# Optimization experiments

Measured on AMD Instinct MI355X. Metric: run time of the kernel, lower is better.

Reference implementation:

```python
import jax, jax.numpy as jnp
import numpy as np

B, L, D, H, M = 4, 2048, 256, 8, 256
HEAD = D // H
EPS = 1e-6


def _pos_embedding(maxlen, d):
    i = np.arange(maxlen, dtype=np.float64)[:, None]
    j = np.arange(d, dtype=np.float64)[None, :]
    angle = i / np.power(10000.0, (j - (j % 2)) / d)
    pe = np.where(j % 2 == 0, np.sin(angle), np.cos(angle))
    return jnp.asarray(pe, jnp.float32)  # [L, D]


def _projection_matrix(m, d, seed=0):
    # FAVOR+ orthogonal random features: one full QR block (m == d here),
    # rows rescaled by norms of iid Gaussian rows (scaling=0 in source).
    rng = np.random.default_rng(seed)
    block = rng.standard_normal((d, d))
    q, _ = np.linalg.qr(block)
    q = q.T[:m]
    mult = np.linalg.norm(rng.standard_normal((m, d)), axis=1)
    return jnp.asarray(mult[:, None] * q, jnp.float32)  # [M, D]


def _softmax_kernel(x, is_query, proj):
    # x: [B, L, H, D], proj: [M, D]
    d = x.shape[-1]
    m = proj.shape[0]
    x = x * (float(d) ** -0.25)
    xp = jnp.einsum('blhd,md->blhm', x, proj)
    diag = 0.5 * jnp.sum(x * x, axis=-1, keepdims=True)
    if is_query:
        mx = jnp.max(xp, axis=-1, keepdims=True)
    else:
        mx = jnp.max(xp, axis=(-3, -1), keepdims=True)  # over L and M
    return (float(m) ** -0.5) * (jnp.exp(xp - diag - mx) + EPS)


def setup_inputs() -> dict:
    key = jax.random.key(0)
    ks = jax.random.split(key, 12)
    s = 1.0 / np.sqrt(D)
    inp = {
        'query': jax.random.normal(ks[0], (B, L, D), jnp.float32),
        'key': jax.random.normal(ks[1], (B, L, D), jnp.float32),
        'value': jax.random.normal(ks[2], (B, L, D), jnp.float32),
        'mask': jnp.ones((B, L), jnp.float32),
        'Wq': jax.random.normal(ks[3], (D, D), jnp.float32) * s,
        'bq': jnp.zeros((D,), jnp.float32),
        'Wk': jax.random.normal(ks[4], (D, D), jnp.float32) * s,
        'bk': jnp.zeros((D,), jnp.float32),
        'Wv': jax.random.normal(ks[5], (D, D), jnp.float32) * s,
        'bv': jnp.zeros((D,), jnp.float32),
        'Wo': jax.random.normal(ks[6], (D, D), jnp.float32) * s,
        'bo': jnp.zeros((D,), jnp.float32),
        'proj': _projection_matrix(M, D, seed=0),
        'pos': _pos_embedding(L, D),
    }
    return inp


def reference(query, key, value, mask, Wq, bq, Wk, bk, Wv, bv, Wo, bo, proj, pos):
    b = query.shape[0]
    q = query @ Wq + bq                      # [B, L, D]
    k = key @ Wk + bk
    v = value @ Wv + bv
    # per-head copies keep the FULL model_size feature dim (as in source)
    q = jnp.broadcast_to(q[:, :, None, :], (b, L, H, D))
    k = jnp.broadcast_to(k[:, :, None, :], (b, L, H, D))
    pos_b = pos[None]                        # [1, L, D]
    cos_pos = jnp.repeat(pos_b[..., None, 1::2], 2, axis=-1)  # [1, L, 1, D]
    sin_pos = jnp.repeat(pos_b[..., None, ::2], 2, axis=-1)

    def rot(x):
        x2 = jnp.stack([-x[..., 1::2], x[..., ::2]], axis=-1).reshape(x.shape)
        return x * cos_pos + x2 * sin_pos

    q = rot(q)
    k = rot(k)
    v = v.reshape(b, L, H, HEAD)

    qp = _softmax_kernel(q, True, proj)      # [B, L, H, M]
    kp = _softmax_kernel(k, False, proj)     # [B, L, H, M]

    kvs = jnp.einsum('blhm,blhd->bhmd', kp, v)
    num = jnp.einsum('blhm,bhmd->blhd', qp, kvs)
    den = jnp.einsum('blhm,bhm->blh', qp, jnp.sum(kp, axis=1))
    ctx = (num / den[..., None]).reshape(b, L, D)
    return ctx @ Wo + bo
```

## Files before the change

### kernel.cpp

```cpp
#include <hip/hip_runtime.h>

typedef unsigned short u16;
typedef unsigned int u32;
typedef __bf16 bf16x8 __attribute__((ext_vector_type(8)));
typedef float f32x4 __attribute__((ext_vector_type(4)));

__device__ __forceinline__ float bf2f(u16 u) { return __uint_as_float(((u32)u) << 16); }
__device__ __forceinline__ u16 f2bf(float f) {
  u32 x = __float_as_uint(f);
  x += 0x7fffu + ((x >> 16) & 1u);
  return (u16)(x >> 16);
}
__device__ __forceinline__ u32 encf(float x) {
  u32 u = __float_as_uint(x);
  return (u >> 31) ? ~u : (u | 0x80000000u);
}
__device__ __forceinline__ float decf(u32 e) {
  return (e >> 31) ? __uint_as_float(e & 0x7fffffffu) : __uint_as_float(~e);
}

#define MFMA(a, b, c) __builtin_amdgcn_mfma_f32_16x16x32_bf16(a, b, c, 0, 0, 0)

__global__ __launch_bounds__(256) void prep_w(
    const float* Wq, const float* Wk, const float* Wv, const float* Wo,
    const float* proj, const float* bv,
    u16* WqT, u16* WkT, u16* projb, u16* WWT, float* bw,
    float* __restrict__ ksum, u32* __restrict__ mxk) {
  __shared__ u16 tsh[32][33];
  __shared__ u16 As[64][40];
  __shared__ u16 Bs[64][40];
  const int z = blockIdx.z;
  const int x = threadIdx.x, y = threadIdx.y;
  const int tid = y * 32 + x;
  if (z < 2) {
    const float* s = z == 0 ? Wq : Wk;
    u16* d = z == 0 ? WqT : WkT;
    int r0 = blockIdx.y * 32, c0 = blockIdx.x * 32;
#pragma unroll
    for (int i = 0; i < 32; i += 8) tsh[y + i][x] = f2bf(s[(r0 + y + i) * 256 + c0 + x]);
    __syncthreads();
#pragma unroll
    for (int i = 0; i < 32; i += 8) d[(c0 + y + i) * 256 + r0 + x] = tsh[x][y + i];
    return;
  }
  if (z == 2) {
    int r0 = blockIdx.y * 32, c0 = blockIdx.x * 32;
#pragma unroll
    for (int i = 0; i < 32; i += 8)
      projb[(r0 + y + i) * 256 + c0 + x] = f2bf(proj[(r0 + y + i) * 256 + c0 + x]);
    return;
  }
  if (blockIdx.x < 4 && blockIdx.y < 4) {
    const int o0 = blockIdx.x * 64, i0 = blockIdx.y * 64;
    const int lane = tid & 63, wid = tid >> 6;
    const int wm = (wid >> 1) * 32, wn = (wid & 1) * 32;
    const int fm = lane & 15, fq = (lane >> 4) * 8, rowq = (lane >> 4) * 4;
    const int dr = tid >> 3, oc = (tid & 7) * 8;
    const int ir = tid >> 2, dc = (tid & 3) * 8;
    f32x4 acc[2][2] = {};
    for (int it = 0; it < 8; ++it) {
      int d0 = it * 32;
      float4 w0 = *(const float4*)(Wo + (d0 + dr) * 256 + o0 + oc);
      float4 w1 = *(const float4*)(Wo + (d0 + dr) * 256 + o0 + oc + 4);
      float4 v0 = *(const float4*)(Wv + (i0 + ir) * 256 + d0 + dc);
      float4 v1 = *(const float4*)(Wv + (i0 + ir) * 256 + d0 + dc + 4);
      __syncthreads();
      float wv[8] = {w0.x, w0.y, w0.z, w0.w, w1.x, w1.y, w1.z, w1.w};
#pragma unroll
      for (int j = 0; j < 8; ++j) As[oc + j][dr] = f2bf(wv[j]);
      u16* bp = &Bs[ir][dc];
      bp[0] = f2bf(v0.x); bp[1] = f2bf(v0.y); bp[2] = f2bf(v0.z); bp[3] = f2bf(v0.w);
      bp[4] = f2bf(v1.x); bp[5] = f2bf(v1.y); bp[6] = f2bf(v1.z); bp[7] = f2bf(v1.w);
      __syncthreads();
      bf16x8 a0 = *(const bf16x8*)&As[wm + fm][fq];
      bf16x8 a1 = *(const bf16x8*)&As[wm + 16 + fm][fq];
      bf16x8 b0 = *(const bf16x8*)&Bs[wn + fm][fq];
      bf16x8 b1 = *(const bf16x8*)&Bs[wn + 16 + fm][fq];
      acc[0][0] = MFMA(a0, b0, acc[0][0]);
      acc[0][1] = MFMA(a0, b1, acc[0][1]);
      acc[1][0] = MFMA(a1, b0, acc[1][0]);
      acc[1][1] = MFMA(a1, b1, acc[1][1]);
    }
#pragma unroll
    for (int mt = 0; mt < 2; ++mt)
#pragma unroll
      for (int nt = 0; nt < 2; ++nt)
#pragma unroll
        for (int r = 0; r < 4; ++r)
          WWT[(o0 + wm + mt * 16 + rowq + r) * 256 + i0 + wn + nt * 16 + fm] =
              f2bf(acc[mt][nt][r]);
    return;
  }
  if (blockIdx.x == 4 && blockIdx.y == 0) {
    float s = 0.0f;
    for (int d = 0; d < 256; ++d) s = fmaf(bv[d], Wo[d * 256 + tid], s);
    bw[tid] = s;
    for (int i = tid; i < 1024; i += 256) ksum[i] = 0.0f;
    if (tid < 4) mxk[tid] = 0u;
  }
}

__global__ __launch_bounds__(256, 2) void projrot2(
    const float* __restrict__ Xq, const float* __restrict__ Xk,
    const u16* __restrict__ WqT, const u16* __restrict__ WkT,
    const float* __restrict__ bq, const float* __restrict__ bk,
    const float* __restrict__ pos, const u16* __restrict__ projb,
    float* __restrict__ diag_k, u16* __restrict__ qp,
    float* __restrict__ xp, u32* __restrict__ mxk) {
  const int mode = blockIdx.z;
  const float* X = mode ? Xq : Xk;
  const u16* W = mode ? WqT : WkT;
  const float* bias = mode ? bq : bk;
  __shared__ u16 As[2][32][40];
  __shared__ u16 Bs[2][256][40];
  __shared__ u16 cbuf[32][264];
  __shared__ float dred[2][32];
  __shared__ float mred[2][32];
  __shared__ float wred[4];
  const int row0 = blockIdx.x * 32;
  const int t = threadIdx.x;
  const int lane = t & 63, wid = t >> 6;
  const int wrow = wid & 1, wcol = wid >> 1;
  const int fm = lane & 15, fq = (lane >> 4) * 8, rowq = (lane >> 4) * 4;
  const int ar = t >> 3, ak = (t & 7) * 4;

  const float* Xr = X + (long long)(row0 + ar) * 256;
  const u16* Wr = W + (long long)t * 256;
  float4 av = *(const float4*)(Xr + ak);
  uint4 bv0 = ((const uint4*)Wr)[0];
  uint4 bv1 = ((const uint4*)Wr)[1];
  uint4 bv2 = ((const uint4*)Wr)[2];
  uint4 bv3 = ((const uint4*)Wr)[3];
  As[0][ar][ak] = f2bf(av.x); As[0][ar][ak + 1] = f2bf(av.y);
  As[0][ar][ak + 2] = f2bf(av.z); As[0][ar][ak + 3] = f2bf(av.w);
  { uint4* bsp = (uint4*)&Bs[0][t][0]; bsp[0] = bv0; bsp[1] = bv1; bsp[2] = bv2; bsp[3] = bv3; }
  av = *(const float4*)(Xr + 32 + ak);
  { const uint4* wn = (const uint4*)(Wr + 32); bv0 = wn[0]; bv1 = wn[1]; bv2 = wn[2]; bv3 = wn[3]; }
  __syncthreads();
  f32x4 acc[8] = {};
  for (int s = 0; s < 8; ++s) {
    const int cur = s & 1;
    float4 av2; uint4 nb0, nb1, nb2, nb3;
    if (s < 6) {
      av2 = *(const float4*)(Xr + (s + 2) * 32 + ak);
      const uint4* wn = (const uint4*)(Wr + (s + 2) * 32);
      nb0 = wn[0]; nb1 = wn[1]; nb2 = wn[2]; nb3 = wn[3];
    }
    bf16x8 af = *(const bf16x8*)&As[cur][wrow * 16 + fm][fq];
#pragma unroll
    for (int j = 0; j < 8; ++j) {
      bf16x8 bf = *(const bf16x8*)&Bs[cur][wcol * 128 + j * 16 + fm][fq];
      acc[j] = MFMA(af, bf, acc[j]);
    }
    if (s < 7) {
      const int nxt = cur ^ 1;
      As[nxt][ar][ak] = f2bf(av.x); As[nxt][ar][ak + 1] = f2bf(av.y);
      As[nxt][ar][ak + 2] = f2bf(av.z); As[nxt][ar][ak + 3] = f2bf(av.w);
      uint4* bsp = (uint4*)&Bs[nxt][t][0];
      bsp[0] = bv0; bsp[1] = bv1; bsp[2] = bv2; bsp[3] = bv3;
      if (s < 6) { av = av2; bv0 = nb0; bv1 = nb1; bv2 = nb2; bv3 = nb3; }
      __syncthreads();
    }
  }

  float dsum[4] = {};
#pragma unroll
  for (int j = 0; j < 8; ++j) {
    float bb2 = bias[wcol * 128 + j * 16 + fm];
#pragma unroll
    for (int r = 0; r < 4; ++r) {
      float v = acc[j][r] + bb2;
      acc[j][r] = v;
      dsum[r] += v * v;
    }
  }
#pragma unroll
  for (int o = 1; o < 16; o <<= 1)
#pragma unroll
    for (int r = 0; r < 4; ++r) dsum[r] += __shfl_xor(dsum[r], o, 64);
  if (fm == 0) {
#pragma unroll
    for (int r = 0; r < 4; ++r) dred[wcol][wrow * 16 + rowq + r] = dsum[r];
  }
  __syncthreads();
  if (mode == 0 && t < 32) diag_k[row0 + t] = 0.03125f * (dred[0][t] + dred[1][t]);

#pragma unroll
  for (int j = 0; j < 8; ++j) {
    const int c = wcol * 128 + j * 16 + fm;
#pragma unroll
    for (int r = 0; r < 4; ++r) {
      const int row = wrow * 16 + rowq + r;
      const int l = (row0 + row) & 2047;
      float v = acc[j][r];
      float prt = __shfl_xor(v, 1, 64);
      float x2 = (fm & 1) ? prt : -prt;
      float2 cs = *(const float2*)(pos + (long long)l * 256 + (c & ~1));
      cbuf[row][c] = f2bf(0.25f * (v * cs.y + x2 * cs.x));
    }
  }

  const u16* Pr = projb + (long long)t * 256;
  uint4 pv0 = ((const uint4*)Pr)[0];
  uint4 pv1 = ((const uint4*)Pr)[1];
  uint4 pv2 = ((const uint4*)Pr)[2];
  uint4 pv3 = ((const uint4*)Pr)[3];
  { uint4* bsp = (uint4*)&Bs[0][t][0]; bsp[0] = pv0; bsp[1] = pv1; bsp[2] = pv2; bsp[3] = pv3; }
  { const uint4* pn = (const uint4*)(Pr + 32); pv0 = pn[0]; pv1 = pn[1]; pv2 = pn[2]; pv3 = pn[3]; }
  __syncthreads();
  f32x4 acc2[8] = {};
  for (int s = 0; s < 8; ++s) {
    const int cur = s & 1;
    uint4 np0, np1, np2, np3;
    if (s < 6) {
      const uint4* pn = (const uint4*)(Pr + (s + 2) * 32);
      np0 = pn[0]; np1 = pn[1]; np2 = pn[2]; np3 = pn[3];
    }
    bf16x8 af = *(const bf16x8*)&cbuf[wrow * 16 + fm][s * 32 + fq];
#pragma unroll
    for (int j = 0; j < 8; ++j) {
      bf16x8 bf = *(const bf16x8*)&Bs[cur][wcol * 128 + j * 16 + fm][fq];
      acc2[j] = MFMA(af, bf, acc2[j]);
    }
    if (s < 7) {
      const int nxt = cur ^ 1;
      uint4* bsp = (uint4*)&Bs[nxt][t][0];
      bsp[0] = pv0; bsp[1] = pv1; bsp[2] = pv2; bsp[3] = pv3;
      if (s < 6) { pv0 = np0; pv1 = np1; pv2 = np2; pv3 = np3; }
      __syncthreads();
    }
  }

  if (mode == 1) {
    float m4[4] = {-3.0e38f, -3.0e38f, -3.0e38f, -3.0e38f};
#pragma unroll
    for (int j = 0; j < 8; ++j)
#pragma unroll
      for (int r = 0; r < 4; ++r) m4[r] = fmaxf(m4[r], acc2[j][r]);
#pragma unroll
    for (int o = 1; o < 16; o <<= 1)
#pragma unroll
      for (int r = 0; r < 4; ++r) m4[r] = fmaxf(m4[r], __shfl_xor(m4[r], o, 64));
    if (fm == 0) {
#pragma unroll
      for (int r = 0; r < 4; ++r) mred[wcol][wrow * 16 + rowq + r] = m4[r];
    }
    __syncthreads();
#pragma unroll
    for (int j = 0; j < 8; ++j) {
      const int col = wcol * 128 + j * 16 + fm;
#pragma unroll
      for (int r = 0; r < 4; ++r) {
        const int row = wrow * 16 + rowq + r;
        float mxr = fmaxf(mred[0][row], mred[1][row]);
        float dgr = 0.03125f * (dred[0][row] + dred[1][row]);
        float v = 0.0625f * (__expf(acc2[j][r] - dgr - mxr) + 1e-6f);
        qp[(long long)(row0 + row) * 256 + col] = f2bf(v);
      }
    }
  } else {
    float mx = -3.0e38f;
#pragma unroll
    for (int j = 0; j < 8; ++j) {
      int col = wcol * 128 + j * 16 + fm;
#pragma unroll
      for (int r = 0; r < 4; ++r) {
        float v = acc2[j][r];
        xp[(long long)(row0 + wrow * 16 + rowq + r) * 256 + col] = v;
        mx = fmaxf(mx, v);
      }
    }
#pragma unroll
    for (int o = 32; o > 0; o >>= 1) mx = fmaxf(mx, __shfl_xor(mx, o, 64));
    if (lane == 0) wred[wid] = mx;
    __syncthreads();
    if (t == 0) {
      float m = fmaxf(fmaxf(wred[0], wred[1]), fmaxf(wred[2], wred[3]));
      atomicMax(mxk + (row0 >> 11), encf(m));
    }
  }
}

__global__ __launch_bounds__(256, 2) void kvs_raw_split(
    const float* __restrict__ xp, const float* __restrict__ Xv,
    const float* __restrict__ diag_k, const u32* __restrict__ mxk,
    float* __restrict__ part, float* __restrict__ ksum) {
  __shared__ u16 As[2][64][40];
  __shared__ u16 Bs[2][64][40];
  __shared__ float ksbuf[32][65];
  const int mxt = blockIdx.x, ny = blockIdx.y, z = blockIdx.z;
  const int b = z >> 3, kc = z & 7;
  const long long l0 = (long long)b * 2048 + kc * 256;
  const int t = threadIdx.x;
  const int lane = t & 63, wid = t >> 6;
  const int wrow = wid >> 1, wcol = wid & 1;
  const int fm = lane & 15, rowq = (lane >> 4) * 4;
  const float mxv = decf(mxk[b]);
  const int sr = t >> 3, sc = (t & 7) * 8;
  const int pcol = (((sr >> 3) ^ (t & 3)) << 3) + (sr & 7);
  const int g = lane >> 4;
  const int arow0 = wrow * 32 + fm, arow1 = arow0 + 16;
  const int brow0 = wcol * 32 + fm, brow1 = brow0 + 16;
  const int apg0 = (g ^ ((arow0 >> 3) & 3)) << 3;
  const int apg1 = (g ^ ((arow1 >> 3) & 3)) << 3;
  const int bpg0 = (g ^ ((brow0 >> 3) & 3)) << 3;
  const int bpg1 = (g ^ ((brow1 >> 3) & 3)) << 3;
  f32x4 acc[2][2] = {};
  float ksp[8] = {};
  long long lrow = l0 + sr;
  float4 x0 = *(const float4*)(xp + lrow * 256 + mxt * 64 + sc);
  float4 x1 = *(const float4*)(xp + lrow * 256 + mxt * 64 + sc + 4);
  float4 v0 = *(const float4*)(Xv + lrow * 256 + ny * 64 + sc);
  float4 v1 = *(const float4*)(Xv + lrow * 256 + ny * 64 + sc + 4);
  float dgl = diag_k[lrow];
  {
    float xv[8] = {x0.x, x0.y, x0.z, x0.w, x1.x, x1.y, x1.z, x1.w};
    float vv[8] = {v0.x, v0.y, v0.z, v0.w, v1.x, v1.y, v1.z, v1.w};
#pragma unroll
    for (int j = 0; j < 8; ++j) {
      float f = 0.0625f * (__expf(xv[j] - dgl - mxv) + 1e-6f);
      u16 kb = f2bf(f);
      As[0][sc + j][pcol] = kb;
      ksp[j] += bf2f(kb);
      Bs[0][sc + j][pcol] = f2bf(vv[j]);
    }
  }
  lrow = l0 + 32 + sr;
  x0 = *(const float4*)(xp + lrow * 256 + mxt * 64 + sc);
  x1 = *(const float4*)(xp + lrow * 256 + mxt * 64 + sc + 4);
  v0 = *(const float4*)(Xv + lrow * 256 + ny * 64 + sc);
  v1 = *(const float4*)(Xv + lrow * 256 + ny * 64 + sc + 4);
  dgl = diag_k[lrow];
  __syncthreads();
  for (int s = 0; s < 8; ++s) {
    const int cur = s & 1;
    float4 nx0, nx1, nv0, nv1; float ndg;
    if (s < 6) {
      long long lr2 = l0 + (s + 2) * 32 + sr;
      nx0 = *(const float4*)(xp + lr2 * 256 + mxt * 64 + sc);
      nx1 = *(const float4*)(xp + lr2 * 256 + mxt * 64 + sc + 4);
      nv0 = *(const float4*)(Xv + lr2 * 256 + ny * 64 + sc);
      nv1 = *(const float4*)(Xv + lr2 * 256 + ny * 64 + sc + 4);
      ndg = diag_k[lr2];
    }
    bf16x8 a0 = *(const bf16x8*)&As[cur][arow0][apg0];
    bf16x8 a1 = *(const bf16x8*)&As[cur][arow1][apg1];
    bf16x8 b0 = *(const bf16x8*)&Bs[cur][brow0][bpg0];
    bf16x8 b1 = *(const bf16x8*)&Bs[cur][brow1][bpg1];
    acc[0][0] = MFMA(a0, b0, acc[0][0]);
    acc[0][1] = MFMA(a0, b1, acc[0][1]);
    acc[1][0] = MFMA(a1, b0, acc[1][0]);
    acc[1][1] = MFMA(a1, b1, acc[1][1]);
    if (s < 7) {
      const int nxt = cur ^ 1;
      float xv[8] = {x0.x, x0.y, x0.z, x0.w, x1.x, x1.y, x1.z, x1.w};
      float vv[8] = {v0.x, v0.y, v0.z, v0.w, v1.x, v1.y, v1.z, v1.w};
#pragma unroll
      for (int j = 0; j < 8; ++j) {
        float f = 0.0625f * (__expf(xv[j] - dgl - mxv) + 1e-6f);
        u16 kb = f2bf(f);
        As[nxt][sc + j][pcol] = kb;
        ksp[j] += bf2f(kb);
        Bs[nxt][sc + j][pcol] = f2bf(vv[j]);
      }
      if (s < 6) { x0 = nx0; x1 = nx1; v0 = nv0; v1 = nv1; dgl = ndg; }
      __syncthreads();
    }
  }
#pragma unroll
  for (int mt = 0; mt < 2; ++mt)
#pragma unroll
    for (int nt = 0; nt < 2; ++nt)
#pragma unroll
      for (int r = 0; r < 4; ++r)
        part[(long long)z * 65536 +
             (long long)(mxt * 64 + wrow * 32 + mt * 16 + rowq + r) * 256 +
             ny * 64 + wcol * 32 + nt * 16 + fm] = acc[mt][nt][r];
#pragma unroll
  for (int j = 0; j < 8; ++j) ksbuf[sr][sc + j] = ksp[j];
  __syncthreads();
  if (ny == 0 && t < 64) {
    float ssum = 0.0f;
    for (int r = 0; r < 32; ++r) ssum += ksbuf[r][t];
    atomicAdd(ksum + b * 256 + mxt * 64 + t, ssum);
  }
}

__global__ __launch_bounds__(256) void kvsw(
    const u16* __restrict__ WWT, const float* __restrict__ part,
    const float* __restrict__ ksum, const float* __restrict__ bw,
    u16* __restrict__ kvsWT) {
  __shared__ u16 As[2][64][40];
  __shared__ u16 Bs[2][16][40];
  const int bid = blockIdx.x;
  const int b = bid >> 6;
  const int o0 = ((bid >> 4) & 3) * 64;
  const int m0 = (bid & 15) * 16;
  const int t = threadIdx.x;
  const int w4 = t >> 6;
  const int lane = t & 63;
  const int fm = lane & 15, fq = (lane >> 4) * 8, rowq = (lane >> 4) * 4;
  const int arow = t >> 2, acol = (t & 3) * 8;
  const int brow = t >> 4, bcol = (t & 15) * 2;
  const float* pbase = part + (long long)(b * 8) * 65536 + (m0 + brow) * 256 + bcol;
  f32x4 acc = {0.0f, 0.0f, 0.0f, 0.0f};
  uint4 av = *(const uint4*)(WWT + (o0 + arow) * 256 + acol);
  float2 ps[8];
#pragma unroll
  for (int kc = 0; kc < 8; ++kc) ps[kc] = *(const float2*)(pbase + (long long)kc * 65536);
  {
    float sx = ps[0].x + ps[1].x + ps[2].x + ps[3].x + ps[4].x + ps[5].x + ps[6].x + ps[7].x;
    float sy = ps[0].y + ps[1].y + ps[2].y + ps[3].y + ps[4].y + ps[5].y + ps[6].y + ps[7].y;
    *(uint4*)&As[0][arow][acol] = av;
    Bs[0][brow][bcol] = f2bf(sx);
    Bs[0][brow][bcol + 1] = f2bf(sy);
  }
  av = *(const uint4*)(WWT + (o0 + arow) * 256 + 32 + acol);
#pragma unroll
  for (int kc = 0; kc < 8; ++kc) ps[kc] = *(const float2*)(pbase + (long long)kc * 65536 + 32);
  __syncthreads();
  for (int s = 0; s < 8; ++s) {
    const int cur = s & 1;
    uint4 nav; float2 nps[8];
    if (s < 6) {
      const int k2 = (s + 2) * 32;
      nav = *(const uint4*)(WWT + (o0 + arow) * 256 + k2 + acol);
#pragma unroll
      for (int kc = 0; kc < 8; ++kc) nps[kc] = *(const float2*)(pbase + (long long)kc * 65536 + k2);
    }
    bf16x8 af = *(const bf16x8*)&As[cur][w4 * 16 + fm][fq];
    bf16x8 bf = *(const bf16x8*)&Bs[cur][fm][fq];
    acc = MFMA(af, bf, acc);
    if (s < 7) {
      const int nxt = cur ^ 1;
      float sx = ps[0].x + ps[1].x + ps[2].x + ps[3].x + ps[4].x + ps[5].x + ps[6].x + ps[7].x;
      float sy = ps[0].y + ps[1].y + ps[2].y + ps[3].y + ps[4].y + ps[5].y + ps[6].y + ps[7].y;
      *(uint4*)&As[nxt][arow][acol] = av;
      Bs[nxt][brow][bcol] = f2bf(sx);
      Bs[nxt][brow][bcol + 1] = f2bf(sy);
      if (s < 6) {
        av = nav;
#pragma unroll
        for (int kc = 0; kc < 8; ++kc) ps[kc] = nps[kc];
      }
      __syncthreads();
    }
  }
  const int col = m0 + fm;
  float ksv = ksum[b * 256 + col];
#pragma unroll
  for (int r = 0; r < 4; ++r) {
    int row = o0 + w4 * 16 + rowq + r;
    kvsWT[(long long)b * 65536 + (long long)row * 256 + col] =
        f2bf(acc[r] + bw[row] * ksv);
  }
}

__global__ __launch_bounds__(256, 2) void numout(
    const u16* __restrict__ qp, const float* __restrict__ ksum,
    const u16* __restrict__ kvsWT, const float* __restrict__ bo,
    float* __restrict__ out) {
  __shared__ u16 As[2][16][40];
  __shared__ u16 Bs[2][256][40];
  __shared__ float ksm[256], dsh[16];
  const int row0 = blockIdx.x * 16;
  const int b = blockIdx.z;
  const long long qrow = (long long)b * 2048 + row0;
  const int t = threadIdx.x;
  const int lane = t & 63, wid = t >> 6;
  const int fm = lane & 15, fq = (lane >> 4) * 8, rowq = (lane >> 4) * 4;
  const int ar = t >> 4, ak = (t & 15) * 2;

  const u16* qa = qp + (qrow + ar) * 256;
  const u16* kvr = kvsWT + (long long)b * 65536 + (long long)t * 256;

  u32 a0 = *(const u32*)(qa + ak);
  uint4 bv0 = ((const uint4*)kvr)[0];
  uint4 bv1 = ((const uint4*)kvr)[1];
  uint4 bv2 = ((const uint4*)kvr)[2];
  uint4 bv3 = ((const uint4*)kvr)[3];
  *(u32*)&As[0][ar][ak] = a0;
  { uint4* bsp = (uint4*)&Bs[0][t][0]; bsp[0] = bv0; bsp[1] = bv1; bsp[2] = bv2; bsp[3] = bv3; }
  a0 = *(const u32*)(qa + 32 + ak);
  { const uint4* kn = (const uint4*)(kvr + 32); bv0 = kn[0]; bv1 = kn[1]; bv2 = kn[2]; bv3 = kn[3]; }

  ksm[t] = ksum[b * 256 + t];
  const int prow = t >> 4, pc0 = (t & 15) * 16;
  const u16* qr = qp + (qrow + prow) * 256 + pc0;
  uint4 u0 = *(const uint4*)(qr);
  uint4 u1 = *(const uint4*)(qr + 8);
  __syncthreads();

  float denp = 0.0f;
  u32 uu[8] = {u0.x, u0.y, u0.z, u0.w, u1.x, u1.y, u1.z, u1.w};
#pragma unroll
  for (int j = 0; j < 8; ++j) {
    denp += bf2f((u16)(uu[j] & 0xffffu)) * ksm[pc0 + 2 * j];
    denp += bf2f((u16)(uu[j] >> 16)) * ksm[pc0 + 2 * j + 1];
  }
#pragma unroll
  for (int o = 1; o < 16; o <<= 1) denp += __shfl_xor(denp, o, 64);
  if ((t & 15) == 0) dsh[prow] = denp;

  f32x4 acc[4] = {};
  for (int s = 0; s < 8; ++s) {
    const int cur = s & 1;
    u32 na0; uint4 nb0, nb1, nb2, nb3;
    if (s < 6) {
      const int k2 = (s + 2) * 32;
      na0 = *(const u32*)(qa + k2 + ak);
      const uint4* kn = (const uint4*)(kvr + k2);
      nb0 = kn[0]; nb1 = kn[1]; nb2 = kn[2]; nb3 = kn[3];
    }
    bf16x8 af = *(const bf16x8*)&As[cur][fm][fq];
#pragma unroll
    for (int j = 0; j < 4; ++j) {
      bf16x8 bf = *(const bf16x8*)&Bs[cur][wid * 64 + j * 16 + fm][fq];
      acc[j] = MFMA(af, bf, acc[j]);
    }
    if (s < 7) {
      const int nxt = cur ^ 1;
      *(u32*)&As[nxt][ar][ak] = a0;
      uint4* bsp = (uint4*)&Bs[nxt][t][0];
      bsp[0] = bv0; bsp[1] = bv1; bsp[2] = bv2; bsp[3] = bv3;
      if (s < 6) { a0 = na0; bv0 = nb0; bv1 = nb1; bv2 = nb2; bv3 = nb3; }
      __syncthreads();
    }
  }
#pragma unroll
  for (int j = 0; j < 4; ++j) {
    int col = wid * 64 + j * 16 + fm;
    float bb2 = bo[col];
#pragma unroll
    for (int r = 0; r < 4; ++r) {
      int l = rowq + r;
      out[(qrow + l) * 256 + col] = acc[j][r] / dsh[l] + bb2;
    }
  }
}

extern "C" void kernel_launch(void* const* d_in, const int* in_sizes, int n_in,
                              void* d_out, int out_size, void* d_ws, size_t ws_size,
                              hipStream_t stream) {
  (void)in_sizes; (void)n_in; (void)out_size; (void)ws_size;
  const float* query = (const float*)d_in[0];
  const float* key = (const float*)d_in[1];
  const float* value = (const float*)d_in[2];
  const float* Wq = (const float*)d_in[4];
  const float* bq = (const float*)d_in[5];
  const float* Wk = (const float*)d_in[6];
  const float* bk = (const float*)d_in[7];
  const float* Wv = (const float*)d_in[8];
  const float* bv = (const float*)d_in[9];
  const float* Wo = (const float*)d_in[10];
  const float* bo = (const float*)d_in[11];
  const float* proj = (const float*)d_in[12];
  const float* pos = (const float*)d_in[13];

  char* w = (char*)d_ws;
  u16* qp = (u16*)(w);
  float* xp = (float*)(w + (4 << 20));
  float* part = (float*)(w + (12 << 20));
  u16* kvsWT = (u16*)(w + (20 << 20));
  u16* WqT = (u16*)(w + (21 << 20));
  u16* WkT = WqT + 65536;
  u16* projb = WkT + 65536;
  u16* WWT = projb + 65536;
  float* diag_k = (float*)(w + (22 << 20));
  float* ksum = diag_k + 8192;
  float* bw = ksum + 1024;
  u32* mxk = (u32*)(bw + 256);

  prep_w<<<dim3(8, 8, 4), dim3(32, 8), 0, stream>>>(Wq, Wk, Wv, Wo, proj, bv,
                                                    WqT, WkT, projb, WWT, bw,
                                                    ksum, mxk);
  projrot2<<<dim3(256, 1, 2), dim3(256), 0, stream>>>(
      query, key, WqT, WkT, bq, bk, pos, projb, diag_k, qp, xp, mxk);
  kvs_raw_split<<<dim3(4, 4, 32), dim3(256), 0, stream>>>(xp, value, diag_k, mxk,
                                                          part, ksum);
  kvsw<<<dim3(256), dim3(256), 0, stream>>>(WWT, part, ksum, bw, kvsWT);
  numout<<<dim3(128, 1, 4), dim3(256), 0, stream>>>(qp, ksum, kvsWT, bo,
                                                    (float*)d_out);
}
```

Measured before the change: 66.57 us.

## Apply fused Wv·Wo to value rows before KV accumulation instead of after

The value projection, pre-multiplied by Wo (WWT), is now applied directly to the value rows as a third mode of the projection kernel and stored as bf16. The KV-state kernel then contracts the key features with these pre-transformed values, with operand roles swapped. The separate kvsw GEMM is replaced by a simple reduction over the split partials plus the bias term. This removes one small GEMM launch and halves the value-read bandwidth through bf16, but it adds a full L×D×D GEMM per batch and an extra bf16 rounding step on the values.

```diff
diff --git a/kernel.cpp b/kernel.cpp
--- a/kernel.cpp
+++ b/kernel.cpp
@@ -102,15 +102,14 @@
 
 __global__ __launch_bounds__(256, 2) void projrot2(
     const float* __restrict__ Xq, const float* __restrict__ Xk,
+    const float* __restrict__ Xv,
     const u16* __restrict__ WqT, const u16* __restrict__ WkT,
+    const u16* __restrict__ WWT,
     const float* __restrict__ bq, const float* __restrict__ bk,
     const float* __restrict__ pos, const u16* __restrict__ projb,
     float* __restrict__ diag_k, u16* __restrict__ qp,
-    float* __restrict__ xp, u32* __restrict__ mxk) {
+    float* __restrict__ xp, u16* __restrict__ xvw, u32* __restrict__ mxk) {
   const int mode = blockIdx.z;
-  const float* X = mode ? Xq : Xk;
-  const u16* W = mode ? WqT : WkT;
-  const float* bias = mode ? bq : bk;
   __shared__ u16 As[2][32][40];
   __shared__ u16 Bs[2][256][40];
   __shared__ u16 cbuf[32][264];
@@ -123,6 +122,9 @@
   const int wrow = wid & 1, wcol = wid >> 1;
   const int fm = lane & 15, fq = (lane >> 4) * 8, rowq = (lane >> 4) * 4;
   const int ar = t >> 3, ak = (t & 7) * 4;
+
+  const float* X = mode == 0 ? Xk : (mode == 1 ? Xq : Xv);
+  const u16* W = mode == 0 ? WkT : (mode == 1 ? WqT : WWT);
 
   const float* Xr = X + (long long)(row0 + ar) * 256;
   const u16* Wr = W + (long long)t * 256;
@@ -163,6 +165,18 @@
     }
   }
 
+  if (mode == 2) {
+#pragma unroll
+    for (int j = 0; j < 8; ++j) {
+      const int col = wcol * 128 + j * 16 + fm;
+#pragma unroll
+      for (int r = 0; r < 4; ++r)
+        xvw[(long long)(row0 + wrow * 16 + rowq + r) * 256 + col] = f2bf(acc[j][r]);
+    }
+    return;
+  }
+
+  const float* bias = mode ? bq : bk;
   float dsum[4] = {};
 #pragma unroll
   for (int j = 0; j < 8; ++j) {
@@ -282,13 +296,13 @@
 }
 
 __global__ __launch_bounds__(256, 2) void kvs_raw_split(
-    const float* __restrict__ xp, const float* __restrict__ Xv,
+    const float* __restrict__ xp, const u16* __restrict__ xvw,
     const float* __restrict__ diag_k, const u32* __restrict__ mxk,
     float* __restrict__ part, float* __restrict__ ksum) {
   __shared__ u16 As[2][64][40];
   __shared__ u16 Bs[2][64][40];
   __shared__ float ksbuf[32][65];
-  const int mxt = blockIdx.x, ny = blockIdx.y, z = blockIdx.z;
+  const int ox = blockIdx.x, my = blockIdx.y, z = blockIdx.z;
   const int b = z >> 3, kc = z & 7;
   const long long l0 = (long long)b * 2048 + kc * 256;
   const int t = threadIdx.x;
@@ -308,39 +322,39 @@
   f32x4 acc[2][2] = {};
   float ksp[8] = {};
   long long lrow = l0 + sr;
-  float4 x0 = *(const float4*)(xp + lrow * 256 + mxt * 64 + sc);
-  float4 x1 = *(const float4*)(xp + lrow * 256 + mxt * 64 + sc + 4);
-  float4 v0 = *(const float4*)(Xv + lrow * 256 + ny * 64 + sc);
-  float4 v1 = *(const float4*)(Xv + lrow * 256 + ny * 64 + sc + 4);
+  uint4 va = *(const uint4*)(xvw + lrow * 256 + ox * 64 + sc);
+  float4 x0 = *(const float4*)(xp + lrow * 256 + my * 64 + sc);
+  float4 x1 = *(const float4*)(xp + lrow * 256 + my * 64 + sc + 4);
   float dgl = diag_k[lrow];
   {
+    u16 a8[8] = {(u16)(va.x & 0xffffu), (u16)(va.x >> 16),
+                 (u16)(va.y & 0xffffu), (u16)(va.y >> 16),
+                 (u16)(va.z & 0xffffu), (u16)(va.z >> 16),
+                 (u16)(va.w & 0xffffu), (u16)(va.w >> 16)};
     float xv[8] = {x0.x, x0.y, x0.z, x0.w, x1.x, x1.y, x1.z, x1.w};
-    float vv[8] = {v0.x, v0.y, v0.z, v0.w, v1.x, v1.y, v1.z, v1.w};
 #pragma unroll
     for (int j = 0; j < 8; ++j) {
+      As[0][sc + j][pcol] = a8[j];
       float f = 0.0625f * (__expf(xv[j] - dgl - mxv) + 1e-6f);
       u16 kb = f2bf(f);
-      As[0][sc + j][pcol] = kb;
+      Bs[0][sc + j][pcol] = kb;
       ksp[j] += bf2f(kb);
-      Bs[0][sc + j][pcol] = f2bf(vv[j]);
     }
   }
   lrow = l0 + 32 + sr;
-  x0 = *(const float4*)(xp + lrow * 256 + mxt * 64 + sc);
-  x1 = *(const float4*)(xp + lrow * 256 + mxt * 64 + sc + 4);
-  v0 = *(const float4*)(Xv + lrow * 256 + ny * 64 + sc);
-  v1 = *(const float4*)(Xv + lrow * 256 + ny * 64 + sc + 4);
+  va = *(const uint4*)(xvw + lrow * 256 + ox * 64 + sc);
+  x0 = *(const float4*)(xp + lrow * 256 + my * 64 + sc);
+  x1 = *(const float4*)(xp + lrow * 256 + my * 64 + sc + 4);
   dgl = diag_k[lrow];
   __syncthreads();
   for (int s = 0; s < 8; ++s) {
     const int cur = s & 1;
-    float4 nx0, nx1, nv0, nv1; float ndg;
+    uint4 nva; float4 nx0, nx1; float ndg;
     if (s < 6) {
       long long lr2 = l0 + (s + 2) * 32 + sr;
-      nx0 = *(const float4*)(xp + lr2 * 256 + mxt * 64 + sc);
-      nx1 = *(const float4*)(xp + lr2 * 256 + mxt * 64 + sc + 4);
-      nv0 = *(const float4*)(Xv + lr2 * 256 + ny * 64 + sc);
-      nv1 = *(const float4*)(Xv + lr2 * 256 + ny * 64 + sc + 4);
+      nva = *(const uint4*)(xvw + lr2 * 256 + ox * 64 + sc);
+      nx0 = *(const float4*)(xp + lr2 * 256 + my * 64 + sc);
+      nx1 = *(const float4*)(xp + lr2 * 256 + my * 64 + sc + 4);
       ndg = diag_k[lr2];
     }
     bf16x8 a0 = *(const bf16x8*)&As[cur][arow0][apg0];
@@ -353,17 +367,20 @@
     acc[1][1] = MFMA(a1, b1, acc[1][1]);
     if (s < 7) {
       const int nxt = cur ^ 1;
+      u16 a8[8] = {(u16)(va.x & 0xffffu), (u16)(va.x >> 16),
+                   (u16)(va.y & 0xffffu), (u16)(va.y >> 16),
+                   (u16)(va.z & 0xffffu), (u16)(va.z >> 16),
+                   (u16)(va.w & 0xffffu), (u16)(va.w >> 16)};
       float xv[8] = {x0.x, x0.y, x0.z, x0.w, x1.x, x1.y, x1.z, x1.w};
-      float vv[8] = {v0.x, v0.y, v0.z, v0.w, v1.x, v1.y, v1.z, v1.w};
 #pragma unroll
       for (int j = 0; j < 8; ++j) {
+        As[nxt][sc + j][pcol] = a8[j];
         float f = 0.0625f * (__expf(xv[j] - dgl - mxv) + 1e-6f);
         u16 kb = f2bf(f);
-        As[nxt][sc + j][pcol] = kb;
+        Bs[nxt][sc + j][pcol] = kb;
         ksp[j] += bf2f(kb);
-        Bs[nxt][sc + j][pcol] = f2bf(vv[j]);
       }
-      if (s < 6) { x0 = nx0; x1 = nx1; v0 = nv0; v1 = nv1; dgl = ndg; }
+      if (s < 6) { va = nva; x0 = nx0; x1 = nx1; dgl = ndg; }
       __syncthreads();
     }
   }
@@ -374,85 +391,34 @@
 #pragma unroll
       for (int r = 0; r < 4; ++r)
         part[(long long)z * 65536 +
-             (long long)(mxt * 64 + wrow * 32 + mt * 16 + rowq + r) * 256 +
-             ny * 64 + wcol * 32 + nt * 16 + fm] = acc[mt][nt][r];
+             (long long)(ox * 64 + wrow * 32 + mt * 16 + rowq + r) * 256 +
+             my * 64 + wcol * 32 + nt * 16 + fm] = acc[mt][nt][r];
 #pragma unroll
   for (int j = 0; j < 8; ++j) ksbuf[sr][sc + j] = ksp[j];
   __syncthreads();
-  if (ny == 0 && t < 64) {
+  if (ox == 0 && t < 64) {
     float ssum = 0.0f;
     for (int r = 0; r < 32; ++r) ssum += ksbuf[r][t];
-    atomicAdd(ksum + b * 256 + mxt * 64 + t, ssum);
-  }
-}
-
-__global__ __launch_bounds__(256) void kvsw(
-    const u16* __restrict__ WWT, const float* __restrict__ part,
-    const float* __restrict__ ksum, const float* __restrict__ bw,
-    u16* __restrict__ kvsWT) {
-  __shared__ u16 As[2][64][40];
-  __shared__ u16 Bs[2][16][40];
-  const int bid = blockIdx.x;
-  const int b = bid >> 6;
-  const int o0 = ((bid >> 4) & 3) * 64;
-  const int m0 = (bid & 15) * 16;
+    atomicAdd(ksum + b * 256 + my * 64 + t, ssum);
+  }
+}
+
+__global__ __launch_bounds__(256) void kvsred(
+    const float* __restrict__ part, const float* __restrict__ ksum,
+    const float* __restrict__ bw, u16* __restrict__ kvsWT) {
+  const int b = blockIdx.z;
+  const int o0 = blockIdx.x * 4;
   const int t = threadIdx.x;
-  const int w4 = t >> 6;
-  const int lane = t & 63;
-  const int fm = lane & 15, fq = (lane >> 4) * 8, rowq = (lane >> 4) * 4;
-  const int arow = t >> 2, acol = (t & 3) * 8;
-  const int brow = t >> 4, bcol = (t & 15) * 2;
-  const float* pbase = part + (long long)(b * 8) * 65536 + (m0 + brow) * 256 + bcol;
-  f32x4 acc = {0.0f, 0.0f, 0.0f, 0.0f};
-  uint4 av = *(const uint4*)(WWT + (o0 + arow) * 256 + acol);
-  float2 ps[8];
-#pragma unroll
-  for (int kc = 0; kc < 8; ++kc) ps[kc] = *(const float2*)(pbase + (long long)kc * 65536);
-  {
-    float sx = ps[0].x + ps[1].x + ps[2].x + ps[3].x + ps[4].x + ps[5].x + ps[6].x + ps[7].x;
-    float sy = ps[0].y + ps[1].y + ps[2].y + ps[3].y + ps[4].y + ps[5].y + ps[6].y + ps[7].y;
-    *(uint4*)&As[0][arow][acol] = av;
-    Bs[0][brow][bcol] = f2bf(sx);
-    Bs[0][brow][bcol + 1] = f2bf(sy);
-  }
-  av = *(const uint4*)(WWT + (o0 + arow) * 256 + 32 + acol);
-#pragma unroll
-  for (int kc = 0; kc < 8; ++kc) ps[kc] = *(const float2*)(pbase + (long long)kc * 65536 + 32);
-  __syncthreads();
-  for (int s = 0; s < 8; ++s) {
-    const int cur = s & 1;
-    uint4 nav; float2 nps[8];
-    if (s < 6) {
-      const int k2 = (s + 2) * 32;
-      nav = *(const uint4*)(WWT + (o0 + arow) * 256 + k2 + acol);
-#pragma unroll
-      for (int kc = 0; kc < 8; ++kc) nps[kc] = *(const float2*)(pbase + (long long)kc * 65536 + k2);
-    }
-    bf16x8 af = *(const bf16x8*)&As[cur][w4 * 16 + fm][fq];
-    bf16x8 bf = *(const bf16x8*)&Bs[cur][fm][fq];
-    acc = MFMA(af, bf, acc);
-    if (s < 7) {
-      const int nxt = cur ^ 1;
-      float sx = ps[0].x + ps[1].x + ps[2].x + ps[3].x + ps[4].x + ps[5].x + ps[6].x + ps[7].x;
-      float sy = ps[0].y + ps[1].y + ps[2].y + ps[3].y + ps[4].y + ps[5].y + ps[6].y + ps[7].y;
-      *(uint4*)&As[nxt][arow][acol] = av;
-      Bs[nxt][brow][bcol] = f2bf(sx);
-      Bs[nxt][brow][bcol + 1] = f2bf(sy);
-      if (s < 6) {
-        av = nav;
-#pragma unroll
-        for (int kc = 0; kc < 8; ++kc) ps[kc] = nps[kc];
-      }
-      __syncthreads();
-    }
-  }
-  const int col = m0 + fm;
-  float ksv = ksum[b * 256 + col];
-#pragma unroll
-  for (int r = 0; r < 4; ++r) {
-    int row = o0 + w4 * 16 + rowq + r;
-    kvsWT[(long long)b * 65536 + (long long)row * 256 + col] =
-        f2bf(acc[r] + bw[row] * ksv);
+  const float ksv = ksum[b * 256 + t];
+#pragma unroll
+  for (int o = 0; o < 4; ++o) {
+    const int orow = o0 + o;
+    const float* pb = part + (long long)(b * 8) * 65536 + (long long)orow * 256 + t;
+    float s = 0.0f;
+#pragma unroll
+    for (int kc = 0; kc < 8; ++kc) s += pb[(long long)kc * 65536];
+    kvsWT[(long long)b * 65536 + (long long)orow * 256 + t] =
+        f2bf(s + bw[orow] * ksv);
   }
 }
 
@@ -560,13 +526,14 @@
   char* w = (char*)d_ws;
   u16* qp = (u16*)(w);
   float* xp = (float*)(w + (4 << 20));
-  float* part = (float*)(w + (12 << 20));
-  u16* kvsWT = (u16*)(w + (20 << 20));
-  u16* WqT = (u16*)(w + (21 << 20));
+  u16* xvw = (u16*)(w + (12 << 20));
+  float* part = (float*)(w + (16 << 20));
+  u16* kvsWT = (u16*)(w + (24 << 20));
+  u16* WqT = (u16*)(w + (25 << 20));
   u16* WkT = WqT + 65536;
   u16* projb = WkT + 65536;
   u16* WWT = projb + 65536;
-  float* diag_k = (float*)(w + (22 << 20));
+  float* diag_k = (float*)(w + (26 << 20));
   float* ksum = diag_k + 8192;
   float* bw = ksum + 1024;
   u32* mxk = (u32*)(bw + 256);
@@ -574,11 +541,12 @@
   prep_w<<<dim3(8, 8, 4), dim3(32, 8), 0, stream>>>(Wq, Wk, Wv, Wo, proj, bv,
                                                     WqT, WkT, projb, WWT, bw,
                                                     ksum, mxk);
-  projrot2<<<dim3(256, 1, 2), dim3(256), 0, stream>>>(
-      query, key, WqT, WkT, bq, bk, pos, projb, diag_k, qp, xp, mxk);
-  kvs_raw_split<<<dim3(4, 4, 32), dim3(256), 0, stream>>>(xp, value, diag_k, mxk,
+  projrot2<<<dim3(256, 1, 3), dim3(256), 0, stream>>>(
+      query, key, value, WqT, WkT, WWT, bq, bk, pos, projb, diag_k, qp, xp,
+      xvw, mxk);
+  kvs_raw_split<<<dim3(4, 4, 32), dim3(256), 0, stream>>>(xp, xvw, diag_k, mxk,
                                                           part, ksum);
-  kvsw<<<dim3(256), dim3(256), 0, stream>>>(WWT, part, ksum, bw, kvsWT);
+  kvsred<<<dim3(64, 1, 4), dim3(256), 0, stream>>>(part, ksum, bw, kvsWT);
   numout<<<dim3(128, 1, 4), dim3(256), 0, stream>>>(qp, ksum, kvsWT, bo,
                                                     (float*)d_out);
 }
```

Result: no change. 66.86 us (+0.4%).
